# Optimization experiments

Measured on AMD Instinct MI355X. Metric: run time of the kernel, lower is better.

Reference implementation:

```python
import jax, jax.numpy as jnp
import numpy as np


def lstm_step(x_t, h, c, Wih, Whh, bih, bhh):
    # PyTorch LSTM gate order: i, f, g, o
    gates = x_t @ Wih.T + h @ Whh.T + bih + bhh
    i, f, g, o = jnp.split(gates, 4, axis=-1)
    i = jax.nn.sigmoid(i)
    f = jax.nn.sigmoid(f)
    g = jnp.tanh(g)
    o = jax.nn.sigmoid(o)
    c_new = f * c + i * g
    h_new = o * jnp.tanh(c_new)
    return h_new, c_new


def setup_inputs() -> dict:
    key = jax.random.key(0)
    N, C, T, V, M = 512, 3, 300, 25, 2
    F = C * V * M  # 150
    H = 100
    ks = jax.random.split(key, 12)
    s = 1.0 / np.sqrt(H)  # PyTorch LSTM/Linear init scale
    u = lambda k, shape: jax.random.uniform(k, shape, jnp.float32, -s, s)
    return {
        "x": jax.random.normal(ks[0], (N, C, T, V, M), jnp.float32),
        "enc_Wih": u(ks[1], (4 * H, F)),
        "enc_Whh": u(ks[2], (4 * H, H)),
        "enc_bih": u(ks[3], (4 * H,)),
        "enc_bhh": u(ks[4], (4 * H,)),
        "dec_Wih": u(ks[5], (4 * H, F)),
        "dec_Whh": u(ks[6], (4 * H, H)),
        "dec_bih": u(ks[7], (4 * H,)),
        "dec_bhh": u(ks[8], (4 * H,)),
        "fc_W": u(ks[9], (F, H)),
        "fc_b": u(ks[10], (F,)),
    }


def reference(x, enc_Wih, enc_Whh, enc_bih, enc_bhh,
              dec_Wih, dec_Whh, dec_bih, dec_bhh, fc_W, fc_b):
    N, C, T, V, M = x.shape
    F = C * V * M
    H = enc_Whh.shape[1]
    # (N,C,T,V,M) -> (N,T,C*V*M)
    xs = jnp.transpose(x, (0, 2, 1, 3, 4)).reshape(N, T, F)

    # Encoder LSTM: only need final (h, c)
    h0 = jnp.zeros((N, H), x.dtype)
    c0 = jnp.zeros((N, H), x.dtype)

    def enc_step(carry, xt):
        h, c = carry
        h, c = lstm_step(xt, h, c, enc_Wih, enc_Whh, enc_bih, enc_bhh)
        return (h, c), None

    (h, c), _ = jax.lax.scan(enc_step, (h0, c0), jnp.swapaxes(xs, 0, 1))

    inp0 = jnp.zeros((N, F), x.dtype)

    def dec_step(carry, _):
        inp, h, c = carry
        h, c = lstm_step(inp, h, c, dec_Wih, dec_Whh, dec_bih, dec_bhh)
        out = h @ fc_W.T + fc_b
        return (out, h, c), out

    _, outs = jax.lax.scan(dec_step, (inp0, h, c), None, length=T - 1)  # [T-1,N,F]

    # outputs[:,0,:] stays zero, like the torch.zeros buffer
    outputs = jnp.concatenate([jnp.zeros((1, N, F), x.dtype), outs], axis=0)  # [T,N,F]
    outputs = jnp.swapaxes(outputs, 0, 1).reshape(N, T, C, V, M)
    return jnp.transpose(outputs, (0, 2, 1, 3, 4))  # (N,C,T,V,M)
```

## Files before the change

### kernel.cpp

```cpp
#include <hip/hip_runtime.h>
#include <hip/hip_fp16.h>


#define B_W2P   0u
#define B_WDP   102400u
#define B_WEP   204800u
#define B_PIH   307200u
#define B_BENC  460800u
#define B_B1    462848u
#define B_BEFF  464896u
#define B_HIST  466944u
#define HIST_STRIDE 29952
#define B_XG    31137792u

typedef _Float16 h2_t __attribute__((ext_vector_type(2)));

#if defined(__has_builtin)
#if __has_builtin(__builtin_amdgcn_fdot2)
#define HAS_FDOT2 1
#endif
#endif

__device__ __forceinline__ float fdot2u(unsigned a, unsigned b, float c) {
#ifdef HAS_FDOT2
  return __builtin_amdgcn_fdot2(__builtin_bit_cast(h2_t, a), __builtin_bit_cast(h2_t, b), c, false);
#else
  float al = __half2float(__ushort_as_half((unsigned short)(a & 0xffffu)));
  float ah = __half2float(__ushort_as_half((unsigned short)(a >> 16)));
  float bl = __half2float(__ushort_as_half((unsigned short)(b & 0xffffu)));
  float bh = __half2float(__ushort_as_half((unsigned short)(b >> 16)));
  return fmaf(ah, bh, fmaf(al, bl, c));
#endif
}

__device__ __forceinline__ unsigned pack2f(float a, float b) {
  return (unsigned)__half_as_ushort(__float2half(a)) |
         ((unsigned)__half_as_ushort(__float2half(b)) << 16);
}

__device__ __forceinline__ float fast_sig(float x) {
  float e = __builtin_amdgcn_exp2f(x * -1.442695040888963f);
  return __builtin_amdgcn_rcpf(1.f + e);
}
__device__ __forceinline__ float fast_tanh(float x) {
  float e = __builtin_amdgcn_exp2f(x * -2.885390081777926f);
  return fmaf(2.f, __builtin_amdgcn_rcpf(1.f + e), -1.f);
}

__device__ __forceinline__ float lstm_tail(float acc, int ty, float& c) {
  float sg = fast_sig(acc);
  float th = fast_tanh(acc);
  float act = (ty == 2) ? th : sg;
  float v1 = __shfl_xor(act, 1);
  float v2 = __shfl_xor(act, 2);
  float v3 = __shfl_xor(v1, 2);
  c = fmaf(v1, c, act * v2);
  return v3 * fast_tanh(c);
}

__device__ __forceinline__ float dot100(const unsigned short* hb, const unsigned* wp) {
  const uint4* h4 = (const uint4*)hb;
  float a0 = 0.f, a1 = 0.f, a2 = 0.f, a3 = 0.f;
#pragma unroll
  for (int ch = 0; ch < 12; ++ch) {
    uint4 v = h4[ch];
    a0 = fdot2u(wp[4 * ch + 0], v.x, a0);
    a1 = fdot2u(wp[4 * ch + 1], v.y, a1);
    a2 = fdot2u(wp[4 * ch + 2], v.z, a2);
    a3 = fdot2u(wp[4 * ch + 3], v.w, a3);
  }
  uint2 v2 = *(const uint2*)(hb + 96);
  a0 = fdot2u(wp[48], v2.x, a0);
  a1 = fdot2u(wp[49], v2.y, a1);
  return (a0 + a1) + (a2 + a3);
}

__global__ void prep(const float* __restrict__ dWih, const float* __restrict__ dWhh,
                     const float* __restrict__ dbih, const float* __restrict__ dbhh,
                     const float* __restrict__ eWih, const float* __restrict__ eWhh,
                     const float* __restrict__ ebih, const float* __restrict__ ebhh,
                     const float* __restrict__ fcW,  const float* __restrict__ fcb,
                     char* __restrict__ wsb)
{
  int idx = blockIdx.x * 256 + threadIdx.x;
  if (idx < 25600) {
    int q = idx >> 9, t = idx & 511;
    unsigned w2p = 0, wdp = 0, wep = 0;
    if (t < 400) {
      int r = (t & 3) * 100 + (t >> 2);
      int j0 = 2 * q, j1 = 2 * q + 1;
      float wd0 = dWhh[r * 100 + j0], wd1 = dWhh[r * 100 + j1];
      float we0 = eWhh[r * 100 + j0], we1 = eWhh[r * 100 + j1];
      float s0 = 0.f, s1 = 0.f;
      for (int f = 0; f < 150; ++f) {
        float a = dWih[r * 150 + f];
        s0 = fmaf(a, fcW[f * 100 + j0], s0);
        s1 = fmaf(a, fcW[f * 100 + j1], s1);
      }
      w2p = pack2f(wd0 + s0, wd1 + s1);
      wdp = pack2f(wd0, wd1);
      wep = pack2f(we0, we1);
    }
    ((unsigned*)(wsb + B_W2P))[idx] = w2p;
    ((unsigned*)(wsb + B_WDP))[idx] = wdp;
    ((unsigned*)(wsb + B_WEP))[idx] = wep;
  } else if (idx < 25600 + 38400) {
    int k = idx - 25600; int d = k >> 9, t = k & 511;
    unsigned pk = 0;
    if (t < 400) {
      int r = (t & 3) * 100 + (t >> 2);
      pk = pack2f(eWih[r * 150 + 2 * d], eWih[r * 150 + 2 * d + 1]);
    }
    ((unsigned*)(wsb + B_PIH))[k] = pk;
  } else if (idx < 25600 + 38400 + 512) {
    int t = idx - (25600 + 38400);
    float be = 0.f, b1 = 0.f, bf = 0.f;
    if (t < 400) {
      int r = (t & 3) * 100 + (t >> 2);
      be = ebih[r] + ebhh[r];
      b1 = dbih[r] + dbhh[r];
      float acc = 0.f;
      for (int f = 0; f < 150; ++f) acc = fmaf(dWih[r * 150 + f], fcb[f], acc);
      bf = b1 + acc;
    }
    ((float*)(wsb + B_BENC))[t] = be;
    ((float*)(wsb + B_B1))[t]   = b1;
    ((float*)(wsb + B_BEFF))[t] = bf;
  }
}

__global__ __launch_bounds__(512, 4)
void pre(const float* __restrict__ x, const char* __restrict__ wsb,
         unsigned short* __restrict__ xg, int tbase)
{
  const int tid = threadIdx.x;
  const int n = blockIdx.x;
  __shared__ unsigned short xls[150 * 160];

  unsigned wih[75];
  const unsigned* pih = (const unsigned*)(wsb + B_PIH);
#pragma unroll
  for (int d = 0; d < 75; ++d) wih[d] = pih[(d << 9) + tid];

  const float* xb = x + (size_t)n * 45000;
  unsigned short* xgr = xg + (size_t)n * 60000 + ((tid < 400) ? tid : 0);
  const bool on = tid < 400;

  for (int d = tid; d < 150 * 160; d += 512) {
    int tl = d / 160, f = d - tl * 160;
    float v = 0.f;
    if (f < 150) {
      int c = f / 50, q = f - c * 50;
      v = xb[c * 15000 + (tbase + tl) * 50 + q];
    }
    xls[tl * 160 + f] = __half_as_ushort(__float2half(v));
  }
  __syncthreads();
  if (on) {
    for (int tl = 0; tl < 150; ++tl) {
      const uint4* row = (const uint4*)(xls + tl * 160);
      float a0 = 0.f, a1 = 0.f, a2 = 0.f, a3 = 0.f;
#pragma unroll
      for (int ch = 0; ch < 18; ++ch) {
        uint4 v = row[ch];
        a0 = fdot2u(wih[4 * ch + 0], v.x, a0);
        a1 = fdot2u(wih[4 * ch + 1], v.y, a1);
        a2 = fdot2u(wih[4 * ch + 2], v.z, a2);
        a3 = fdot2u(wih[4 * ch + 3], v.w, a3);
      }
      uint4 v = row[18];
      a0 = fdot2u(wih[72], v.x, a0);
      a1 = fdot2u(wih[73], v.y, a1);
      a2 = fdot2u(wih[74], v.z, a2);
      float a = (a0 + a1) + (a2 + a3);
      xgr[(size_t)tl * 400] = __half_as_ushort(__float2half(a));
    }
  }
}

__global__ __launch_bounds__(512, 4)
void recurrent(const unsigned short* __restrict__ xg, char* __restrict__ wsb, int phase)
{
  const int t  = threadIdx.x;
  const int n  = blockIdx.x;
  const int j  = t >> 2, ty = t & 3;
  const bool leader = (t < 400) && (ty == 0);
  __shared__ unsigned short hh[2][112];

  const unsigned* WEP = (const unsigned*)(wsb + B_WEP);
  const unsigned* WDP = (const unsigned*)(wsb + B_WDP);
  const unsigned* W2P = (const unsigned*)(wsb + B_W2P);

  unsigned wp[50];
#pragma unroll
  for (int q = 0; q < 50; ++q) wp[q] = WEP[(q << 9) + t];

  const float benc = ((const float*)(wsb + B_BENC))[t];
  const float b1g  = ((const float*)(wsb + B_B1))[t];
  const float beff = ((const float*)(wsb + B_BEFF))[t];
  unsigned short* histn = (unsigned short*)(wsb + B_HIST) + (size_t)n * HIST_STRIDE;
  float* stc = (float*)(histn + 128);
  const unsigned short* xgr = xg + (size_t)n * 60000 + ((t < 400) ? t : 0);
  float c = 0.f;

  if (phase == 0) {
    unsigned short p1 = xgr[400];
    {
      float acc = benc + __half2float(__ushort_as_half(xgr[0]));
      float hn = lstm_tail(acc, ty, c);
      if (leader) hh[1][j] = __half_as_ushort(__float2half(hn));
      __syncthreads();
    }
    for (int ts = 1; ts < 150; ++ts) {
      const int rd = ts & 1, wr = rd ^ 1;
      unsigned short pn = xgr[(size_t)((ts + 1 < 150) ? ts + 1 : 149) * 400];
      float acc = benc + __half2float(__ushort_as_half(p1)) + dot100(hh[rd], wp);
      float hn = lstm_tail(acc, ty, c);
      if (leader) hh[wr][j] = __half_as_ushort(__float2half(hn));
      __syncthreads();
      p1 = pn;
    }
    if (t < 100) histn[t] = hh[0][t];
    if (leader)  stc[j] = c;
    return;
  }

  if (t < 100) hh[0][t] = histn[t];
  if (t < 400) c = stc[j];
  unsigned short p1 = xgr[0];
  __syncthreads();

  for (int ts = 150; ts < 300; ++ts) {
    const int rd = ts & 1, wr = rd ^ 1;
    const int idx = ts - 150;
    unsigned short pn = xgr[(size_t)((idx + 1 < 150) ? idx + 1 : 149) * 400];
    float acc = benc + __half2float(__ushort_as_half(p1)) + dot100(hh[rd], wp);
    float hn = lstm_tail(acc, ty, c);
    if (leader) hh[wr][j] = __half_as_ushort(__float2half(hn));
    __syncthreads();
    p1 = pn;
  }

#pragma unroll
  for (int q = 0; q < 50; ++q) wp[q] = WDP[(q << 9) + t];
  {
    float acc = b1g + dot100(hh[0], wp);
    float hn = lstm_tail(acc, ty, c);
    if (leader) {
      hh[1][j] = __half_as_ushort(__float2half(hn));
      histn[j] = __half_as_ushort(__float2half(hn));
    }
    __syncthreads();
  }
#pragma unroll
  for (int q = 0; q < 50; ++q) wp[q] = W2P[(q << 9) + t];
  for (int s = 2; s <= 299; ++s) {
    const int rd = (299 + s) & 1, wr = rd ^ 1;
    float acc = beff + dot100(hh[rd], wp);
    float hn = lstm_tail(acc, ty, c);
    if (leader) {
      hh[wr][j] = __half_as_ushort(__float2half(hn));
      histn[(s - 1) * 100 + j] = __half_as_ushort(__float2half(hn));
    }
    __syncthreads();
  }
}

__global__ __launch_bounds__(192, 4)
void emit(const char* __restrict__ wsb, const float* __restrict__ fcW,
          const float* __restrict__ fcb, float* __restrict__ out)
{
  const int f = threadIdx.x;
  const int n = blockIdx.x;
  const int z = blockIdx.y;
  __shared__ unsigned short hl[15008];

  const uint4* src = (const uint4*)((const unsigned short*)(wsb + B_HIST) +
                                    (size_t)n * HIST_STRIDE + z * 15000);
  for (int k = f; k < 1875; k += 192) ((uint4*)hl)[k] = src[k];

  const bool on = f < 150;
  unsigned fw[50];
  float bias = 0.f;
  if (on) {
    const float* fp = fcW + f * 100;
#pragma unroll
    for (int q = 0; q < 50; ++q) fw[q] = pack2f(fp[2 * q], fp[2 * q + 1]);
    bias = fcb[f];
  }
  __syncthreads();

  if (!on) return;
  const int cc = f / 50, r = f - cc * 50;
  float* ob = out + (size_t)n * 45000 + cc * 15000 + r;
  if (z == 0) ob[0] = 0.f;
  const int rows = z ? 149 : 150;
  for (int tl = 0; tl < rows; ++tl) {
    const uint4* row = (const uint4*)(hl + tl * 100);
    float a0 = bias, a1 = 0.f, a2 = 0.f, a3 = 0.f;
#pragma unroll
    for (int ch = 0; ch < 12; ++ch) {
      uint4 v = row[ch];
      a0 = fdot2u(fw[4 * ch + 0], v.x, a0);
      a1 = fdot2u(fw[4 * ch + 1], v.y, a1);
      a2 = fdot2u(fw[4 * ch + 2], v.z, a2);
      a3 = fdot2u(fw[4 * ch + 3], v.w, a3);
    }
    uint2 v2 = *(const uint2*)(hl + tl * 100 + 96);
    a0 = fdot2u(fw[48], v2.x, a0);
    a1 = fdot2u(fw[49], v2.y, a1);
    const int tt = z * 150 + tl + 1;
    ob[tt * 50] = (a0 + a1) + (a2 + a3);
  }
}

extern "C" void kernel_launch(void* const* d_in, const int* in_sizes, int n_in,
                              void* d_out, int out_size, void* d_ws, size_t ws_size,
                              hipStream_t stream) {
  const float* x    = (const float*)d_in[0];
  const float* eWih = (const float*)d_in[1];
  const float* eWhh = (const float*)d_in[2];
  const float* ebih = (const float*)d_in[3];
  const float* ebhh = (const float*)d_in[4];
  const float* dWih = (const float*)d_in[5];
  const float* dWhh = (const float*)d_in[6];
  const float* dbih = (const float*)d_in[7];
  const float* dbhh = (const float*)d_in[8];
  const float* fcW  = (const float*)d_in[9];
  const float* fcb  = (const float*)d_in[10];
  float* out = (float*)d_out;
  char* wsb  = (char*)d_ws;

  unsigned short* xg = (unsigned short*)(wsb + B_XG);

  prep<<<252, 256, 0, stream>>>(dWih, dWhh, dbih, dbhh, eWih, eWhh, ebih, ebhh, fcW, fcb, wsb);
  pre<<<512, 512, 0, stream>>>(x, wsb, xg, 0);
  recurrent<<<512, 512, 0, stream>>>(xg, wsb, 0);
  pre<<<512, 512, 0, stream>>>(x, wsb, xg, 150);
  recurrent<<<512, 512, 0, stream>>>(xg, wsb, 1);
  emit<<<dim3(512, 2), 192, 0, stream>>>(wsb, fcW, fcb, out);
}
```

Measured before the change: 1.219 ms.

## Compute all four LSTM gates per thread, cutting recurrent blocks to 128 threads

The recurrent kernel now gives each hidden unit to one thread that computes all four gate dot products (200 packed weight registers as uint4), instead of four threads each computing one gate and exchanging results with shuffles. The block shrinks from 512 to 128 threads, and the xg input prefetch is deepened to two steps. This removes the cross-lane shuffles and uses fewer waves per block, so barriers cost less. In exchange each thread carries four times the dot-product work per step and far more registers, and because the layout reads packed weights as uint4, it depends on prep producing that interleave.

```diff
diff --git a/kernel.cpp b/kernel.cpp
--- a/kernel.cpp
+++ b/kernel.cpp
@@ -47,32 +47,55 @@
   return fmaf(2.f, __builtin_amdgcn_rcpf(1.f + e), -1.f);
 }
 
-__device__ __forceinline__ float lstm_tail(float acc, int ty, float& c) {
-  float sg = fast_sig(acc);
-  float th = fast_tanh(acc);
-  float act = (ty == 2) ? th : sg;
-  float v1 = __shfl_xor(act, 1);
-  float v2 = __shfl_xor(act, 2);
-  float v3 = __shfl_xor(v1, 2);
-  c = fmaf(v1, c, act * v2);
-  return v3 * fast_tanh(c);
-}
-
-__device__ __forceinline__ float dot100(const unsigned short* hb, const unsigned* wp) {
+__device__ __forceinline__ float cell_update(float4 a, float& c) {
+  float i = fast_sig(a.x), f = fast_sig(a.y);
+  float g = fast_tanh(a.z), o = fast_sig(a.w);
+  c = fmaf(f, c, i * g);
+  return o * fast_tanh(c);
+}
+
+__device__ __forceinline__ float4 dot4(const unsigned short* hb, const uint4 (&wq)[50]) {
+  float ai0 = 0.f, af0 = 0.f, ag0 = 0.f, ao0 = 0.f;
+  float ai1 = 0.f, af1 = 0.f, ag1 = 0.f, ao1 = 0.f;
   const uint4* h4 = (const uint4*)hb;
-  float a0 = 0.f, a1 = 0.f, a2 = 0.f, a3 = 0.f;
 #pragma unroll
   for (int ch = 0; ch < 12; ++ch) {
-    uint4 v = h4[ch];
-    a0 = fdot2u(wp[4 * ch + 0], v.x, a0);
-    a1 = fdot2u(wp[4 * ch + 1], v.y, a1);
-    a2 = fdot2u(wp[4 * ch + 2], v.z, a2);
-    a3 = fdot2u(wp[4 * ch + 3], v.w, a3);
-  }
-  uint2 v2 = *(const uint2*)(hb + 96);
-  a0 = fdot2u(wp[48], v2.x, a0);
-  a1 = fdot2u(wp[49], v2.y, a1);
-  return (a0 + a1) + (a2 + a3);
+    uint4 hv = h4[ch];
+    ai0 = fdot2u(wq[4 * ch + 0].x, hv.x, ai0);
+    af0 = fdot2u(wq[4 * ch + 0].y, hv.x, af0);
+    ag0 = fdot2u(wq[4 * ch + 0].z, hv.x, ag0);
+    ao0 = fdot2u(wq[4 * ch + 0].w, hv.x, ao0);
+    ai1 = fdot2u(wq[4 * ch + 1].x, hv.y, ai1);
+    af1 = fdot2u(wq[4 * ch + 1].y, hv.y, af1);
+    ag1 = fdot2u(wq[4 * ch + 1].z, hv.y, ag1);
+    ao1 = fdot2u(wq[4 * ch + 1].w, hv.y, ao1);
+    ai0 = fdot2u(wq[4 * ch + 2].x, hv.z, ai0);
+    af0 = fdot2u(wq[4 * ch + 2].y, hv.z, af0);
+    ag0 = fdot2u(wq[4 * ch + 2].z, hv.z, ag0);
+    ao0 = fdot2u(wq[4 * ch + 2].w, hv.z, ao0);
+    ai1 = fdot2u(wq[4 * ch + 3].x, hv.w, ai1);
+    af1 = fdot2u(wq[4 * ch + 3].y, hv.w, af1);
+    ag1 = fdot2u(wq[4 * ch + 3].z, hv.w, ag1);
+    ao1 = fdot2u(wq[4 * ch + 3].w, hv.w, ao1);
+  }
+  uint2 hv2 = *(const uint2*)(hb + 96);
+  ai0 = fdot2u(wq[48].x, hv2.x, ai0);
+  af0 = fdot2u(wq[48].y, hv2.x, af0);
+  ag0 = fdot2u(wq[48].z, hv2.x, ag0);
+  ao0 = fdot2u(wq[48].w, hv2.x, ao0);
+  ai1 = fdot2u(wq[49].x, hv2.y, ai1);
+  af1 = fdot2u(wq[49].y, hv2.y, af1);
+  ag1 = fdot2u(wq[49].z, hv2.y, ag1);
+  ao1 = fdot2u(wq[49].w, hv2.y, ao1);
+  return make_float4(ai0 + ai1, af0 + af1, ag0 + ag1, ao0 + ao1);
+}
+
+__device__ __forceinline__ float4 unp4(uint2 u) {
+  return make_float4(
+      __half2float(__ushort_as_half((unsigned short)(u.x & 0xffffu))),
+      __half2float(__ushort_as_half((unsigned short)(u.x >> 16))),
+      __half2float(__ushort_as_half((unsigned short)(u.y & 0xffffu))),
+      __half2float(__ushort_as_half((unsigned short)(u.y >> 16))));
 }
 
 __global__ void prep(const float* __restrict__ dWih, const float* __restrict__ dWhh,
@@ -178,88 +201,105 @@
   }
 }
 
-__global__ __launch_bounds__(512, 4)
+__global__ __launch_bounds__(128)
 void recurrent(const unsigned short* __restrict__ xg, char* __restrict__ wsb, int phase)
 {
-  const int t  = threadIdx.x;
-  const int n  = blockIdx.x;
-  const int j  = t >> 2, ty = t & 3;
-  const bool leader = (t < 400) && (ty == 0);
+  const int j = threadIdx.x;
+  const int n = blockIdx.x;
+  const int jj = (j < 100) ? j : 0;
+  const bool act = j < 100;
   __shared__ unsigned short hh[2][112];
 
   const unsigned* WEP = (const unsigned*)(wsb + B_WEP);
   const unsigned* WDP = (const unsigned*)(wsb + B_WDP);
   const unsigned* W2P = (const unsigned*)(wsb + B_W2P);
 
-  unsigned wp[50];
-#pragma unroll
-  for (int q = 0; q < 50; ++q) wp[q] = WEP[(q << 9) + t];
-
-  const float benc = ((const float*)(wsb + B_BENC))[t];
-  const float b1g  = ((const float*)(wsb + B_B1))[t];
-  const float beff = ((const float*)(wsb + B_BEFF))[t];
+  uint4 wq[50];
+#pragma unroll
+  for (int q = 0; q < 50; ++q) wq[q] = ((const uint4*)(WEP + (q << 9)))[j];
+
+  const float4 benc4 = ((const float4*)(wsb + B_BENC))[j];
   unsigned short* histn = (unsigned short*)(wsb + B_HIST) + (size_t)n * HIST_STRIDE;
   float* stc = (float*)(histn + 128);
-  const unsigned short* xgr = xg + (size_t)n * 60000 + ((t < 400) ? t : 0);
+  const unsigned short* xr = xg + (size_t)n * 60000 + 4 * jj;
   float c = 0.f;
+  float hn = 0.f;
 
   if (phase == 0) {
-    unsigned short p1 = xgr[400];
+    uint2 xA = *(const uint2*)(xr);
+    uint2 xB = *(const uint2*)(xr + 400);
     {
-      float acc = benc + __half2float(__ushort_as_half(xgr[0]));
-      float hn = lstm_tail(acc, ty, c);
-      if (leader) hh[1][j] = __half_as_ushort(__float2half(hn));
+      float4 xf = unp4(xA);
+      float4 a = make_float4(benc4.x + xf.x, benc4.y + xf.y,
+                             benc4.z + xf.z, benc4.w + xf.w);
+      hn = cell_update(a, c);
+      if (act) hh[1][j] = __half_as_ushort(__float2half(hn));
       __syncthreads();
+      xA = xB;
+      xB = *(const uint2*)(xr + 2 * 400);
     }
     for (int ts = 1; ts < 150; ++ts) {
-      const int rd = ts & 1, wr = rd ^ 1;
-      unsigned short pn = xgr[(size_t)((ts + 1 < 150) ? ts + 1 : 149) * 400];
-      float acc = benc + __half2float(__ushort_as_half(p1)) + dot100(hh[rd], wp);
-      float hn = lstm_tail(acc, ty, c);
-      if (leader) hh[wr][j] = __half_as_ushort(__float2half(hn));
+      uint2 xN = *(const uint2*)(xr + (size_t)((ts + 2 < 150) ? ts + 2 : 149) * 400);
+      float4 a = dot4(hh[ts & 1], wq);
+      float4 xf = unp4(xA);
+      a.x += benc4.x + xf.x; a.y += benc4.y + xf.y;
+      a.z += benc4.z + xf.z; a.w += benc4.w + xf.w;
+      hn = cell_update(a, c);
+      if (act) hh[(ts & 1) ^ 1][j] = __half_as_ushort(__float2half(hn));
       __syncthreads();
-      p1 = pn;
-    }
-    if (t < 100) histn[t] = hh[0][t];
-    if (leader)  stc[j] = c;
+      xA = xB; xB = xN;
+    }
+    if (act) {
+      histn[j] = __half_as_ushort(__float2half(hn));
+      stc[j] = c;
+    }
     return;
   }
 
-  if (t < 100) hh[0][t] = histn[t];
-  if (t < 400) c = stc[j];
-  unsigned short p1 = xgr[0];
+  if (act) {
+    hh[0][j] = histn[j];
+    c = stc[j];
+  }
+  uint2 xA = *(const uint2*)(xr);
+  uint2 xB = *(const uint2*)(xr + 400);
   __syncthreads();
 
   for (int ts = 150; ts < 300; ++ts) {
-    const int rd = ts & 1, wr = rd ^ 1;
-    const int idx = ts - 150;
-    unsigned short pn = xgr[(size_t)((idx + 1 < 150) ? idx + 1 : 149) * 400];
-    float acc = benc + __half2float(__ushort_as_half(p1)) + dot100(hh[rd], wp);
-    float hn = lstm_tail(acc, ty, c);
-    if (leader) hh[wr][j] = __half_as_ushort(__float2half(hn));
+    const int li = ts - 150;
+    uint2 xN = *(const uint2*)(xr + (size_t)((li + 2 < 150) ? li + 2 : 149) * 400);
+    float4 a = dot4(hh[ts & 1], wq);
+    float4 xf = unp4(xA);
+    a.x += benc4.x + xf.x; a.y += benc4.y + xf.y;
+    a.z += benc4.z + xf.z; a.w += benc4.w + xf.w;
+    hn = cell_update(a, c);
+    if (act) hh[(ts & 1) ^ 1][j] = __half_as_ushort(__float2half(hn));
     __syncthreads();
-    p1 = pn;
-  }
-
-#pragma unroll
-  for (int q = 0; q < 50; ++q) wp[q] = WDP[(q << 9) + t];
+    xA = xB; xB = xN;
+  }
+
+  const float4 b14 = ((const float4*)(wsb + B_B1))[j];
+#pragma unroll
+  for (int q = 0; q < 50; ++q) wq[q] = ((const uint4*)(WDP + (q << 9)))[j];
   {
-    float acc = b1g + dot100(hh[0], wp);
-    float hn = lstm_tail(acc, ty, c);
-    if (leader) {
+    float4 a = dot4(hh[0], wq);
+    a.x += b14.x; a.y += b14.y; a.z += b14.z; a.w += b14.w;
+    hn = cell_update(a, c);
+    if (act) {
       hh[1][j] = __half_as_ushort(__float2half(hn));
       histn[j] = __half_as_ushort(__float2half(hn));
     }
     __syncthreads();
   }
-#pragma unroll
-  for (int q = 0; q < 50; ++q) wp[q] = W2P[(q << 9) + t];
+  const float4 beff4 = ((const float4*)(wsb + B_BEFF))[j];
+#pragma unroll
+  for (int q = 0; q < 50; ++q) wq[q] = ((const uint4*)(W2P + (q << 9)))[j];
   for (int s = 2; s <= 299; ++s) {
-    const int rd = (299 + s) & 1, wr = rd ^ 1;
-    float acc = beff + dot100(hh[rd], wp);
-    float hn = lstm_tail(acc, ty, c);
-    if (leader) {
-      hh[wr][j] = __half_as_ushort(__float2half(hn));
+    const int rd = (299 + s) & 1;
+    float4 a = dot4(hh[rd], wq);
+    a.x += beff4.x; a.y += beff4.y; a.z += beff4.z; a.w += beff4.w;
+    hn = cell_update(a, c);
+    if (act) {
+      hh[rd ^ 1][j] = __half_as_ushort(__float2half(hn));
       histn[(s - 1) * 100 + j] = __half_as_ushort(__float2half(hn));
     }
     __syncthreads();
@@ -335,8 +375,8 @@
 
   prep<<<252, 256, 0, stream>>>(dWih, dWhh, dbih, dbhh, eWih, eWhh, ebih, ebhh, fcW, fcb, wsb);
   pre<<<512, 512, 0, stream>>>(x, wsb, xg, 0);
-  recurrent<<<512, 512, 0, stream>>>(xg, wsb, 0);
+  recurrent<<<512, 128, 0, stream>>>(xg, wsb, 0);
   pre<<<512, 512, 0, stream>>>(x, wsb, xg, 150);
-  recurrent<<<512, 512, 0, stream>>>(xg, wsb, 1);
+  recurrent<<<512, 128, 0, stream>>>(xg, wsb, 1);
   emit<<<dim3(512, 2), 192, 0, stream>>>(wsb, fcW, fcb, out);
 }
```

Result: slower. 3.450 ms (+183.0%).

## Batch 16 samples per block and compute LSTM recurrence with MFMA

Applied to the files above, without the earlier changes.

The recurrent kernel now processes 16 sequences per 320-thread block instead of one sequence per 512-thread block. It replaces the per-thread fdot2 dot products and shuffle-based gate exchange with 16x16x32 f16 MFMA tiles, so each lane ends up holding all four gates of a hidden unit. Weights are gathered into MFMA A-fragments in registers. The hidden state is kept transposed in LDS, and xg inputs are prefetched two steps ahead. Only 32 blocks are launched, so most CUs sit idle; the bet is that the serial per-step latency drops enough to make up for that.

```diff
diff --git a/kernel.cpp b/kernel.cpp
--- a/kernel.cpp
+++ b/kernel.cpp
@@ -14,6 +14,8 @@
 #define B_XG    31137792u
 
 typedef _Float16 h2_t __attribute__((ext_vector_type(2)));
+typedef _Float16 f16x8 __attribute__((ext_vector_type(8)));
+typedef float f32x4v __attribute__((ext_vector_type(4)));
 
 #if defined(__has_builtin)
 #if __has_builtin(__builtin_amdgcn_fdot2)
@@ -47,32 +49,34 @@
   return fmaf(2.f, __builtin_amdgcn_rcpf(1.f + e), -1.f);
 }
 
-__device__ __forceinline__ float lstm_tail(float acc, int ty, float& c) {
-  float sg = fast_sig(acc);
-  float th = fast_tanh(acc);
-  float act = (ty == 2) ? th : sg;
-  float v1 = __shfl_xor(act, 1);
-  float v2 = __shfl_xor(act, 2);
-  float v3 = __shfl_xor(v1, 2);
-  c = fmaf(v1, c, act * v2);
-  return v3 * fast_tanh(c);
-}
-
-__device__ __forceinline__ float dot100(const unsigned short* hb, const unsigned* wp) {
-  const uint4* h4 = (const uint4*)hb;
-  float a0 = 0.f, a1 = 0.f, a2 = 0.f, a3 = 0.f;
-#pragma unroll
-  for (int ch = 0; ch < 12; ++ch) {
-    uint4 v = h4[ch];
-    a0 = fdot2u(wp[4 * ch + 0], v.x, a0);
-    a1 = fdot2u(wp[4 * ch + 1], v.y, a1);
-    a2 = fdot2u(wp[4 * ch + 2], v.z, a2);
-    a3 = fdot2u(wp[4 * ch + 3], v.w, a3);
-  }
-  uint2 v2 = *(const uint2*)(hb + 96);
-  a0 = fdot2u(wp[48], v2.x, a0);
-  a1 = fdot2u(wp[49], v2.y, a1);
-  return (a0 + a1) + (a2 + a3);
+__device__ __forceinline__ float4 unp4(uint2 u) {
+  return make_float4(
+      __half2float(__ushort_as_half((unsigned short)(u.x & 0xffffu))),
+      __half2float(__ushort_as_half((unsigned short)(u.x >> 16))),
+      __half2float(__ushort_as_half((unsigned short)(u.y & 0xffffu))),
+      __half2float(__ushort_as_half((unsigned short)(u.y >> 16))));
+}
+
+__device__ __forceinline__ f32x4v mfma16(uint4 a, uint4 b, f32x4v c) {
+  return __builtin_amdgcn_mfma_f32_16x16x32_f16(
+      __builtin_bit_cast(f16x8, a), __builtin_bit_cast(f16x8, b), c, 0, 0, 0);
+}
+
+__device__ __forceinline__ void gatherA(const unsigned* W, int w, int s, int q,
+                                        uint4 (&af)[5][4]) {
+#pragma unroll
+  for (int i = 0; i < 5; ++i) {
+    const int col = (5 * w + i) * 16 + s;
+#pragma unroll
+    for (int kk = 0; kk < 4; ++kk) {
+      const int q0 = kk * 16 + q * 4;
+      unsigned e0 = (q0 + 0 < 50) ? W[(q0 + 0) * 512 + col] : 0u;
+      unsigned e1 = (q0 + 1 < 50) ? W[(q0 + 1) * 512 + col] : 0u;
+      unsigned e2 = (q0 + 2 < 50) ? W[(q0 + 2) * 512 + col] : 0u;
+      unsigned e3 = (q0 + 3 < 50) ? W[(q0 + 3) * 512 + col] : 0u;
+      af[i][kk] = make_uint4(e0, e1, e2, e3);
+    }
+  }
 }
 
 __global__ void prep(const float* __restrict__ dWih, const float* __restrict__ dWhh,
@@ -178,89 +182,193 @@
   }
 }
 
-__global__ __launch_bounds__(512, 4)
+__global__ __launch_bounds__(320)
 void recurrent(const unsigned short* __restrict__ xg, char* __restrict__ wsb, int phase)
 {
-  const int t  = threadIdx.x;
-  const int n  = blockIdx.x;
-  const int j  = t >> 2, ty = t & 3;
-  const bool leader = (t < 400) && (ty == 0);
-  __shared__ unsigned short hh[2][112];
+  const int tid  = threadIdx.x;
+  const int w    = tid >> 6;
+  const int lane = tid & 63;
+  const int s    = lane & 15;
+  const int q    = lane >> 4;
+  const int nb   = blockIdx.x * 16;
+  const int n    = nb + s;
+
+  __shared__ unsigned short hT[2][16][136];
+
+  for (int k = tid; k < 2 * 16 * 136; k += 320) ((unsigned short*)hT)[k] = 0;
 
   const unsigned* WEP = (const unsigned*)(wsb + B_WEP);
   const unsigned* WDP = (const unsigned*)(wsb + B_WDP);
   const unsigned* W2P = (const unsigned*)(wsb + B_W2P);
 
-  unsigned wp[50];
-#pragma unroll
-  for (int q = 0; q < 50; ++q) wp[q] = WEP[(q << 9) + t];
-
-  const float benc = ((const float*)(wsb + B_BENC))[t];
-  const float b1g  = ((const float*)(wsb + B_B1))[t];
-  const float beff = ((const float*)(wsb + B_BEFF))[t];
+  uint4 af[5][4];
+  gatherA(WEP, w, s, q, af);
+
+  int cells[5];
+  float4 be[5];
+#pragma unroll
+  for (int i = 0; i < 5; ++i) {
+    cells[i] = 4 * (5 * w + i) + q;
+    be[i] = ((const float4*)(wsb + B_BENC))[cells[i]];
+  }
+
   unsigned short* histn = (unsigned short*)(wsb + B_HIST) + (size_t)n * HIST_STRIDE;
-  float* stc = (float*)(histn + 128);
-  const unsigned short* xgr = xg + (size_t)n * 60000 + ((t < 400) ? t : 0);
-  float c = 0.f;
+  float* stcn = (float*)(histn + 128);
+  const unsigned short* xrow = xg + (size_t)n * 60000;
+  int xco[5];
+#pragma unroll
+  for (int i = 0; i < 5; ++i) xco[i] = 4 * cells[i];
+
+  float cst[5] = {0.f, 0.f, 0.f, 0.f, 0.f};
+  float hl[5]  = {0.f, 0.f, 0.f, 0.f, 0.f};
 
   if (phase == 0) {
-    unsigned short p1 = xgr[400];
-    {
-      float acc = benc + __half2float(__ushort_as_half(xgr[0]));
-      float hn = lstm_tail(acc, ty, c);
-      if (leader) hh[1][j] = __half_as_ushort(__float2half(hn));
+    __syncthreads();
+    uint2 xA[5], xB[5];
+#pragma unroll
+    for (int i = 0; i < 5; ++i) {
+      xA[i] = *(const uint2*)(xrow + 0 * 400 + xco[i]);
+      xB[i] = *(const uint2*)(xrow + 1 * 400 + xco[i]);
+    }
+    for (int ts = 0; ts < 150; ++ts) {
+      const int rd = ts & 1;
+      const int tn = (ts + 2 < 150) ? ts + 2 : 149;
+      uint2 xN[5];
+#pragma unroll
+      for (int i = 0; i < 5; ++i) xN[i] = *(const uint2*)(xrow + (size_t)tn * 400 + xco[i]);
+      f32x4v acc[5];
+#pragma unroll
+      for (int i = 0; i < 5; ++i) {
+        float4 xf = unp4(xA[i]);
+        acc[i][0] = be[i].x + xf.x; acc[i][1] = be[i].y + xf.y;
+        acc[i][2] = be[i].z + xf.z; acc[i][3] = be[i].w + xf.w;
+      }
+#pragma unroll
+      for (int kk = 0; kk < 4; ++kk) {
+        uint4 b = *(const uint4*)(&hT[rd][s][kk * 32 + q * 8]);
+#pragma unroll
+        for (int i = 0; i < 5; ++i) acc[i] = mfma16(af[i][kk], b, acc[i]);
+      }
+#pragma unroll
+      for (int i = 0; i < 5; ++i) {
+        float ii = fast_sig(acc[i][0]), ff = fast_sig(acc[i][1]);
+        float gg = fast_tanh(acc[i][2]), oo = fast_sig(acc[i][3]);
+        cst[i] = fmaf(ff, cst[i], ii * gg);
+        hl[i] = oo * fast_tanh(cst[i]);
+        hT[rd ^ 1][s][cells[i]] = __half_as_ushort(__float2half(hl[i]));
+      }
       __syncthreads();
-    }
-    for (int ts = 1; ts < 150; ++ts) {
-      const int rd = ts & 1, wr = rd ^ 1;
-      unsigned short pn = xgr[(size_t)((ts + 1 < 150) ? ts + 1 : 149) * 400];
-      float acc = benc + __half2float(__ushort_as_half(p1)) + dot100(hh[rd], wp);
-      float hn = lstm_tail(acc, ty, c);
-      if (leader) hh[wr][j] = __half_as_ushort(__float2half(hn));
-      __syncthreads();
-      p1 = pn;
-    }
-    if (t < 100) histn[t] = hh[0][t];
-    if (leader)  stc[j] = c;
+#pragma unroll
+      for (int i = 0; i < 5; ++i) { xA[i] = xB[i]; xB[i] = xN[i]; }
+    }
+#pragma unroll
+    for (int i = 0; i < 5; ++i) {
+      histn[cells[i]] = __half_as_ushort(__float2half(hl[i]));
+      stcn[cells[i]]  = cst[i];
+    }
     return;
   }
 
-  if (t < 100) hh[0][t] = histn[t];
-  if (t < 400) c = stc[j];
-  unsigned short p1 = xgr[0];
   __syncthreads();
+#pragma unroll
+  for (int i = 0; i < 5; ++i) {
+    hT[0][s][cells[i]] = histn[cells[i]];
+    cst[i] = stcn[cells[i]];
+  }
+  uint2 xA[5], xB[5];
+#pragma unroll
+  for (int i = 0; i < 5; ++i) {
+    xA[i] = *(const uint2*)(xrow + 0 * 400 + xco[i]);
+    xB[i] = *(const uint2*)(xrow + 1 * 400 + xco[i]);
+  }
+  __syncthreads();
 
   for (int ts = 150; ts < 300; ++ts) {
-    const int rd = ts & 1, wr = rd ^ 1;
-    const int idx = ts - 150;
-    unsigned short pn = xgr[(size_t)((idx + 1 < 150) ? idx + 1 : 149) * 400];
-    float acc = benc + __half2float(__ushort_as_half(p1)) + dot100(hh[rd], wp);
-    float hn = lstm_tail(acc, ty, c);
-    if (leader) hh[wr][j] = __half_as_ushort(__float2half(hn));
+    const int rd = ts & 1;
+    const int li = ts - 150;
+    const int tn = (li + 2 < 150) ? li + 2 : 149;
+    uint2 xN[5];
+#pragma unroll
+    for (int i = 0; i < 5; ++i) xN[i] = *(const uint2*)(xrow + (size_t)tn * 400 + xco[i]);
+    f32x4v acc[5];
+#pragma unroll
+    for (int i = 0; i < 5; ++i) {
+      float4 xf = unp4(xA[i]);
+      acc[i][0] = be[i].x + xf.x; acc[i][1] = be[i].y + xf.y;
+      acc[i][2] = be[i].z + xf.z; acc[i][3] = be[i].w + xf.w;
+    }
+#pragma unroll
+    for (int kk = 0; kk < 4; ++kk) {
+      uint4 b = *(const uint4*)(&hT[rd][s][kk * 32 + q * 8]);
+#pragma unroll
+      for (int i = 0; i < 5; ++i) acc[i] = mfma16(af[i][kk], b, acc[i]);
+    }
+#pragma unroll
+    for (int i = 0; i < 5; ++i) {
+      float ii = fast_sig(acc[i][0]), ff = fast_sig(acc[i][1]);
+      float gg = fast_tanh(acc[i][2]), oo = fast_sig(acc[i][3]);
+      cst[i] = fmaf(ff, cst[i], ii * gg);
+      float h = oo * fast_tanh(cst[i]);
+      hT[rd ^ 1][s][cells[i]] = __half_as_ushort(__float2half(h));
+    }
     __syncthreads();
-    p1 = pn;
-  }
-
-#pragma unroll
-  for (int q = 0; q < 50; ++q) wp[q] = WDP[(q << 9) + t];
+#pragma unroll
+    for (int i = 0; i < 5; ++i) { xA[i] = xB[i]; xB[i] = xN[i]; }
+  }
+
+  gatherA(WDP, w, s, q, af);
+  float4 bb[5];
+#pragma unroll
+  for (int i = 0; i < 5; ++i) bb[i] = ((const float4*)(wsb + B_B1))[cells[i]];
   {
-    float acc = b1g + dot100(hh[0], wp);
-    float hn = lstm_tail(acc, ty, c);
-    if (leader) {
-      hh[1][j] = __half_as_ushort(__float2half(hn));
-      histn[j] = __half_as_ushort(__float2half(hn));
+    f32x4v acc[5];
+#pragma unroll
+    for (int i = 0; i < 5; ++i) {
+      acc[i][0] = bb[i].x; acc[i][1] = bb[i].y;
+      acc[i][2] = bb[i].z; acc[i][3] = bb[i].w;
+    }
+#pragma unroll
+    for (int kk = 0; kk < 4; ++kk) {
+      uint4 b = *(const uint4*)(&hT[0][s][kk * 32 + q * 8]);
+#pragma unroll
+      for (int i = 0; i < 5; ++i) acc[i] = mfma16(af[i][kk], b, acc[i]);
+    }
+#pragma unroll
+    for (int i = 0; i < 5; ++i) {
+      float ii = fast_sig(acc[i][0]), ff = fast_sig(acc[i][1]);
+      float gg = fast_tanh(acc[i][2]), oo = fast_sig(acc[i][3]);
+      cst[i] = fmaf(ff, cst[i], ii * gg);
+      float h = oo * fast_tanh(cst[i]);
+      hT[1][s][cells[i]] = __half_as_ushort(__float2half(h));
+      histn[cells[i]] = __half_as_ushort(__float2half(h));
     }
     __syncthreads();
   }
-#pragma unroll
-  for (int q = 0; q < 50; ++q) wp[q] = W2P[(q << 9) + t];
-  for (int s = 2; s <= 299; ++s) {
-    const int rd = (299 + s) & 1, wr = rd ^ 1;
-    float acc = beff + dot100(hh[rd], wp);
-    float hn = lstm_tail(acc, ty, c);
-    if (leader) {
-      hh[wr][j] = __half_as_ushort(__float2half(hn));
-      histn[(s - 1) * 100 + j] = __half_as_ushort(__float2half(hn));
+  gatherA(W2P, w, s, q, af);
+#pragma unroll
+  for (int i = 0; i < 5; ++i) bb[i] = ((const float4*)(wsb + B_BEFF))[cells[i]];
+  for (int st = 2; st <= 299; ++st) {
+    const int rd = (299 + st) & 1;
+    f32x4v acc[5];
+#pragma unroll
+    for (int i = 0; i < 5; ++i) {
+      acc[i][0] = bb[i].x; acc[i][1] = bb[i].y;
+      acc[i][2] = bb[i].z; acc[i][3] = bb[i].w;
+    }
+#pragma unroll
+    for (int kk = 0; kk < 4; ++kk) {
+      uint4 b = *(const uint4*)(&hT[rd][s][kk * 32 + q * 8]);
+#pragma unroll
+      for (int i = 0; i < 5; ++i) acc[i] = mfma16(af[i][kk], b, acc[i]);
+    }
+#pragma unroll
+    for (int i = 0; i < 5; ++i) {
+      float ii = fast_sig(acc[i][0]), ff = fast_sig(acc[i][1]);
+      float gg = fast_tanh(acc[i][2]), oo = fast_sig(acc[i][3]);
+      cst[i] = fmaf(ff, cst[i], ii * gg);
+      float h = oo * fast_tanh(cst[i]);
+      hT[rd ^ 1][s][cells[i]] = __half_as_ushort(__float2half(h));
+      histn[(st - 1) * 100 + cells[i]] = __half_as_ushort(__float2half(h));
     }
     __syncthreads();
   }
@@ -335,8 +443,8 @@
 
   prep<<<252, 256, 0, stream>>>(dWih, dWhh, dbih, dbhh, eWih, eWhh, ebih, ebhh, fcW, fcb, wsb);
   pre<<<512, 512, 0, stream>>>(x, wsb, xg, 0);
-  recurrent<<<512, 512, 0, stream>>>(xg, wsb, 0);
+  recurrent<<<32, 320, 0, stream>>>(xg, wsb, 0);
   pre<<<512, 512, 0, stream>>>(x, wsb, xg, 150);
-  recurrent<<<512, 512, 0, stream>>>(xg, wsb, 1);
+  recurrent<<<32, 320, 0, stream>>>(xg, wsb, 1);
   emit<<<dim3(512, 2), 192, 0, stream>>>(wsb, fcW, fcb, out);
 }
```

After: 1.357 ms. +11.3%, slower.
